# Kernel tuning notes

Measured on AMD Instinct MI355X. Metric: run time of the kernel, lower is better.

Reference implementation:

```python
import jax, jax.numpy as jnp
import numpy as np
from jax import lax

BBOX_XFORM_CLIP = float(np.log(1000.0 / 16.0))
PRE_NMS_TOP_K = 1000
SCORE_THRESH = 0.05
IOU_THRESH = 0.5
MAX_DET = 100


def _decode_boxes(encoded, anchors):
    # encoded [...,4] = [dy,dx,dh,dw] with weights [10,10,5,5]; anchors [...,4] = [y1,x1,y2,x2]
    dy = encoded[..., 0] / 10.0
    dx = encoded[..., 1] / 10.0
    dh = jnp.minimum(encoded[..., 2] / 5.0, BBOX_XFORM_CLIP)
    dw = jnp.minimum(encoded[..., 3] / 5.0, BBOX_XFORM_CLIP)
    ah = anchors[..., 2] - anchors[..., 0]
    aw = anchors[..., 3] - anchors[..., 1]
    ayc = anchors[..., 0] + 0.5 * ah
    axc = anchors[..., 1] + 0.5 * aw
    yc = dy * ah + ayc
    xc = dx * aw + axc
    h = jnp.exp(dh) * ah
    w = jnp.exp(dw) * aw
    return jnp.stack([yc - 0.5 * h, xc - 0.5 * w, yc + 0.5 * h, xc + 0.5 * w], axis=-1)


def _clip_boxes(boxes, image_shape):
    # boxes [B,N,4]; image_shape [B,2] = (height, width)
    h = image_shape[..., 0:1]
    w = image_shape[..., 1:2]
    maxlen = jnp.concatenate([h, w, h, w], axis=-1)[:, None, :]  # [B,1,4]
    return jnp.clip(boxes, 0.0, maxlen)


def _nms_keep(boxes):
    # Greedy sequential NMS on score-sorted boxes [k,4]; returns keep mask [k].
    k = boxes.shape[0]
    y1, x1, y2, x2 = boxes[:, 0], boxes[:, 1], boxes[:, 2], boxes[:, 3]
    area = (y2 - y1) * (x2 - x1)
    idxs = jnp.arange(k)

    def body(keep, i):
        iy1 = jnp.maximum(y1[i], y1)
        ix1 = jnp.maximum(x1[i], x1)
        iy2 = jnp.minimum(y2[i], y2)
        ix2 = jnp.minimum(x2[i], x2)
        inter = jnp.maximum(iy2 - iy1, 0.0) * jnp.maximum(ix2 - ix1, 0.0)
        union = area[i] + area - inter
        iou = inter / jnp.where(union > 0, union, 1.0)
        suppressed = jnp.any(keep & (idxs < i) & (iou > IOU_THRESH))
        return keep.at[i].set(~suppressed), None

    keep, _ = lax.scan(body, jnp.zeros((k,), jnp.bool_), idxs)
    return keep


def _nms_single(boxes, scores):
    # boxes [k,4], scores [k] sorted descending; mirrors sorted_non_max_suppression_padded output.
    keep = _nms_keep(lax.stop_gradient(boxes))
    valid = keep & jnp.any(boxes > 0, axis=-1)  # zeroed (filtered) boxes never count
    sel = jnp.where(valid, scores, -jnp.inf)
    top_s, top_i = lax.top_k(sel, MAX_DET)
    out_valid = top_s > -jnp.inf
    out_scores = jnp.where(out_valid, top_s, 0.0)
    out_boxes = boxes[top_i] * out_valid[:, None].astype(boxes.dtype)
    return out_scores, out_boxes


def setup_inputs() -> dict:
    key = jax.random.key(0)
    k1, k2, k3, k4 = jax.random.split(key, 4)
    B, K, C = 8, 8192, 91
    raw_boxes = jax.random.normal(k1, (B, K, C * 4), jnp.float32) * 0.5
    raw_scores = jax.random.normal(k2, (B, K, C), jnp.float32) * 2.0
    # valid anchors [y1,x1,y2,x2] inside a 1024x1024 image
    ctr = jax.random.uniform(k3, (B, K, 2), jnp.float32, 0.0, 1024.0)
    sz = jax.random.uniform(k4, (B, K, 2), jnp.float32, 16.0, 128.0)
    anchor_boxes = jnp.concatenate([ctr - 0.5 * sz, ctr + 0.5 * sz], axis=-1)
    image_shape = jnp.full((B, 2), 1024.0, jnp.float32)
    return {"raw_boxes": raw_boxes, "raw_scores": raw_scores,
            "anchor_boxes": anchor_boxes, "image_shape": image_shape}


def reference(raw_boxes, raw_scores, anchor_boxes, image_shape):
    B, K, C = raw_scores.shape
    Cc = C - 1  # background removed

    probs = jax.nn.softmax(raw_scores, axis=-1)[:, :, 1:]           # [B,K,Cc]
    boxes = raw_boxes.reshape(B, K, C, 4)[:, :, 1:, :]              # [B,K,Cc,4]
    anch = jnp.broadcast_to(anchor_boxes[:, :, None, :], boxes.shape)
    dec = _decode_boxes(boxes.reshape(B, K * Cc, 4), anch.reshape(B, K * Cc, 4))
    dec = _clip_boxes(dec, image_shape).reshape(B, K, Cc, 4)

    # per-class top-k pre-NMS candidates (_select_top_k_scores + gather)
    k = min(K, PRE_NMS_TOP_K)
    s_t = jnp.transpose(probs, (0, 2, 1))                           # [B,Cc,K]
    top_s, top_i = lax.top_k(s_t, k)                                # [B,Cc,k]
    b_t = jnp.transpose(dec, (0, 2, 1, 3))                          # [B,Cc,K,4]
    top_b = jnp.take_along_axis(b_t, top_i[..., None], axis=2)      # [B,Cc,k,4]

    # filter_boxes_by_scores: score -> -1, box -> 0 below threshold
    mask = top_s > SCORE_THRESH
    top_s = jnp.where(mask, top_s, -1.0)
    top_b = top_b * mask[..., None].astype(top_b.dtype)

    nms_s, nms_b = jax.vmap(jax.vmap(_nms_single))(top_b, top_s)    # [B,Cc,MAX_DET], [B,Cc,MAX_DET,4]
    classes = jnp.broadcast_to(jnp.arange(Cc, dtype=jnp.int32)[None, :, None], nms_s.shape)

    all_s = nms_s.reshape(B, Cc * MAX_DET)
    all_b = nms_b.reshape(B, Cc * MAX_DET, 4)
    all_c = classes.reshape(B, Cc * MAX_DET)

    fin_s, fin_i = lax.top_k(all_s, MAX_DET)
    fin_b = jnp.take_along_axis(all_b, fin_i[..., None], axis=1)
    fin_c = jnp.take_along_axis(all_c, fin_i, axis=1) + 1           # restore background offset
    num = jnp.sum((fin_s > -1.0).astype(jnp.int32), axis=1)
    return fin_b, fin_s, fin_c, num
```

## Files before the change

### kernel.cpp

```cpp
#include <hip/hip_runtime.h>
#include <stdint.h>

typedef unsigned long long ull;

#define K_ANCH   8192
#define NCLS     91
#define NCC      90
#define B_SZ     8
#define CAP      1024
#define PRE_NMS  1000
#define MAXDET   100
#define CHUNK    128
#define NWMAX    16
#define NBW      128
#define SCORE_TH 0.05f
#define IOU_TH   0.5f
#define BBOX_CLIP 4.1351665565490723f

__device__ __forceinline__ float wave_max64(float v) {
  #pragma unroll
  for (int off = 32; off > 0; off >>= 1) v = fmaxf(v, __shfl_xor(v, off, 64));
  return v;
}
__device__ __forceinline__ float wave_sum64(float v) {
  #pragma unroll
  for (int off = 32; off > 0; off >>= 1) v += __shfl_xor(v, off, 64);
  return v;
}

__device__ __forceinline__ float4 decode_clip(float4 e, float4 a, float imh, float imw) {
#pragma clang fp contract(off)
  float dy = e.x / 10.0f;
  float dx = e.y / 10.0f;
  float dh = fminf(e.z / 5.0f, BBOX_CLIP);
  float dw = fminf(e.w / 5.0f, BBOX_CLIP);
  float ah = a.z - a.x;
  float aw = a.w - a.y;
  float ayc = a.x + 0.5f * ah;
  float axc = a.y + 0.5f * aw;
  float yc = dy * ah + ayc;
  float xc = dx * aw + axc;
  float h = expf(dh) * ah;
  float w = expf(dw) * aw;
  float y1 = yc - 0.5f * h, x1 = xc - 0.5f * w;
  float y2 = yc + 0.5f * h, x2 = xc + 0.5f * w;
  y1 = fminf(fmaxf(y1, 0.0f), imh);
  x1 = fminf(fmaxf(x1, 0.0f), imw);
  y2 = fminf(fmaxf(y2, 0.0f), imh);
  x2 = fminf(fmaxf(x2, 0.0f), imw);
  return make_float4(y1, x1, y2, x2);
}

__device__ __forceinline__ bool iou_gt(float4 bi, float ai, float4 bj, float aj) {
#pragma clang fp contract(off)
  float iy1 = fmaxf(bi.x, bj.x);
  float ix1 = fmaxf(bi.y, bj.y);
  float iy2 = fminf(bi.z, bj.z);
  float ix2 = fminf(bi.w, bj.w);
  float inter = fmaxf(iy2 - iy1, 0.0f) * fmaxf(ix2 - ix1, 0.0f);
  float uni = ai + aj - inter;
  float iou = inter / (uni > 0.0f ? uni : 1.0f);
  return iou > IOU_TH;
}

__global__ __launch_bounds__(256) void kT_softmax(
    const float* __restrict__ raw_scores,
    float2* __restrict__ stats, ull* __restrict__ bmask)
{
  __shared__ ull rowbits[64][2];
  int tid = threadIdx.x;
  int wv = tid >> 6, lane = tid & 63;
  int b = blockIdx.x >> 7;
  int k0 = (blockIdx.x & 127) << 6;
  for (int i = 0; i < 16; i++) {
    int rl = (wv << 4) + i;
    int row = b * K_ANCH + k0 + rl;
    const float* srow = raw_scores + (size_t)row * NCLS;
    float s0 = srow[lane];
    bool has1 = lane < (NCLS - 64);
    float s1 = has1 ? srow[64 + lane] : -INFINITY;
    float m = wave_max64(fmaxf(s0, s1));
    float e0 = expf(s0 - m);
    float e1 = has1 ? expf(s1 - m) : 0.0f;
    float denom = wave_sum64(e0 + e1);
    ull b0 = __ballot(lane >= 1 && (e0 / denom) > SCORE_TH);
    ull b1 = __ballot(has1 && (e1 / denom) > SCORE_TH);
    if (lane == 0) {
      stats[row] = make_float2(m, denom);
      rowbits[rl][0] = b0;
      rowbits[rl][1] = b1;
    }
  }
  __syncthreads();
  if (tid < NCC) {
    int c = tid + 1, w = c >> 6, bit = c & 63;
    ull out = 0;
    for (int r = 0; r < 64; r++)
      out |= ((rowbits[r][w] >> bit) & 1ull) << r;
    bmask[(size_t)(b * NCC + tid) * NBW + (k0 >> 6)] = out;
  }
}

__global__ __launch_bounds__(256) void kN_nms(
    const float* __restrict__ raw_boxes, const float* __restrict__ raw_scores,
    const float* __restrict__ anchors, const float* __restrict__ image_shape,
    const float2* __restrict__ stats, const ull* __restrict__ bmask,
    float* __restrict__ all_s, float4* __restrict__ all_b)
{
  __shared__ ull    skey[CAP];
  __shared__ float4 sbox[PRE_NMS];
  __shared__ float  sarea[PRE_NMS];
  __shared__ ull    smask[NWMAX][CHUNK + 1];
  __shared__ int    soff[NBW];
  __shared__ int    s_n;
  __shared__ int    s_done;

  int bc  = blockIdx.x;
  int tid = threadIdx.x;
  int b = bc / NCC;
  int c = bc - b * NCC + 1;
  int outbase = bc * MAXDET;

  for (int i = tid; i < MAXDET; i += 256) {
    all_s[outbase + i] = 0.0f;
    all_b[outbase + i] = make_float4(0.f, 0.f, 0.f, 0.f);
  }

  ull w0 = 0;
  if (tid < NBW) {
    w0 = bmask[(size_t)bc * NBW + tid];
    soff[tid] = __popcll(w0);
  }
  if (tid == 0) s_done = 0;
  __syncthreads();
  if (tid == 0) {
    int acc = 0;
    for (int t = 0; t < NBW; t++) { int v = soff[t]; soff[t] = acc; acc += v; }
    s_n = acc;
  }
  __syncthreads();
  int n_load = min(s_n, CAP);

  if (tid < NBW) {
    int slot = soff[tid];
    ull m = w0;
    int kb = tid << 6;
    while (m) {
      int bit = __ffsll(m) - 1;
      m &= m - 1;
      if (slot < CAP) skey[slot] = (ull)(kb + bit);
      slot++;
    }
  }
  __syncthreads();

  size_t rowb = (size_t)b * K_ANCH;
  for (int i = tid; i < n_load; i += 256) {
    int k = (int)skey[i];
    size_t row = rowb + k;
    float s = raw_scores[row * NCLS + c];
    float2 md = stats[row];
    float p = expf(s - md.x) / md.y;
    skey[i] = ((ull)__float_as_uint(p) << 32) | (uint32_t)(K_ANCH - 1 - k);
  }
  int n2 = 256;
  while (n2 < n_load) n2 <<= 1;
  for (int i = n_load + tid; i < n2; i += 256) skey[i] = 0ull;
  __syncthreads();

  for (int size = 2; size <= n2; size <<= 1) {
    for (int stride = size >> 1; stride > 0; stride >>= 1) {
      for (int i = tid; i < n2; i += 256) {
        int j = i ^ stride;
        if (j > i) {
          ull ki = skey[i], kj = skey[j];
          bool desc = ((i & size) == 0);
          if (desc ? (ki < kj) : (ki > kj)) { skey[i] = kj; skey[j] = ki; }
        }
      }
      __syncthreads();
    }
  }

  int n_use = min(n_load, PRE_NMS);
  float imh = image_shape[b * 2 + 0];
  float imw = image_shape[b * 2 + 1];
  for (int i = tid; i < n_use; i += 256) {
    int k = K_ANCH - 1 - (int)(skey[i] & 0xFFFFFFFFull);
    size_t row = rowb + k;
    float4 e = ((const float4*)raw_boxes)[row * NCLS + c];
    float4 a = ((const float4*)anchors)[row];
    float4 box = decode_clip(e, a, imh, imw);
    sbox[i] = box;
    {
#pragma clang fp contract(off)
      sarea[i] = (box.z - box.x) * (box.w - box.y);
    }
  }

  int nwords = (n_use + 63) >> 6;
  ull rem = 0;
  int written = 0;
  for (int c0 = 0; c0 < n_use; c0 += CHUNK) {
    __syncthreads();
    if (s_done) break;
    int nrows = min(CHUNK, n_use - c0);

    for (int p = tid; p < (nwords << 7); p += 256) {
      int w  = p >> 7;
      int rr = p & (CHUNK - 1);
      if (rr >= nrows) continue;
      int r = c0 + rr;
      float4 br = sbox[r];
      float  ar = sarea[r];
      int j0 = w << 6;
      int j1 = min(j0 + 64, n_use);
      int js = max(j0, r + 1);
      ull mrow = 0;
      for (int j = js; j < j1; j++) {
        if (iou_gt(br, ar, sbox[j], sarea[j])) mrow |= 1ull << (j - j0);
      }
      smask[w][rr] = mrow;
    }
    __syncthreads();

    if (tid < 64) {
      int lane = tid;
      for (int i = c0; i < c0 + nrows; i++) {
        int w = i >> 6, bit = i & 63;
        ull rw = __shfl(rem, w, 64);
        if (((rw >> bit) & 1ull) == 0) {
          if (lane < nwords) rem |= smask[lane][i - c0];
          int valid = 0;
          float4 bx;
          float sc = 0.f;
          if (lane == 0) {
            bx = sbox[i];
            valid = (bx.x > 0.f || bx.y > 0.f || bx.z > 0.f || bx.w > 0.f) ? 1 : 0;
            sc = __uint_as_float((uint32_t)(skey[i] >> 32));
          }
          valid = __shfl(valid, 0, 64);
          if (valid) {
            if (lane == 0) {
              all_s[outbase + written] = sc;
              all_b[outbase + written] = bx;
            }
            written++;
            if (written == MAXDET) {
              if (lane == 0) s_done = 1;
              break;
            }
          }
        }
      }
    }
  }
}

__global__ __launch_bounds__(256) void k3_final(
    const float* __restrict__ all_s, const float4* __restrict__ all_b,
    float* __restrict__ out)
{
  __shared__ float ss[NCC * MAXDET];
  int b = blockIdx.x;
  int tid = threadIdx.x;
  const float* S = all_s + (size_t)b * NCC * MAXDET;
  for (int i = tid; i < NCC * MAXDET; i += 256) ss[i] = S[i];
  __syncthreads();
  if (tid >= 64) return;
  int lane = tid;

  float* fin_b = out;
  float* fin_s = out + B_SZ * MAXDET * 4;
  float* fin_c = fin_s + B_SZ * MAXDET;
  float* numo  = fin_c + B_SZ * MAXDET;

  int c0 = lane;
  int c1 = lane + 64;
  int p0 = 0, p1 = 0;
  ull k0 = ((ull)__float_as_uint(ss[c0 * MAXDET]) << 32) | (uint32_t)(16383 - c0 * MAXDET);
  ull k1 = (c1 < NCC)
         ? (((ull)__float_as_uint(ss[c1 * MAXDET]) << 32) | (uint32_t)(16383 - c1 * MAXDET))
         : 0ull;
  int cnt = 0;

  for (int step = 0; step < MAXDET; step++) {
    ull my = (k0 > k1) ? k0 : k1;
    ull g = my;
    #pragma unroll
    for (int off = 32; off > 0; off >>= 1) {
      ull o = __shfl_xor(g, off, 64);
      g = (o > g) ? o : g;
    }
    if (g == k0 && k0 != 0ull) {
      p0++;
      int flat = c0 * MAXDET + p0;
      k0 = (p0 < MAXDET)
         ? (((ull)__float_as_uint(ss[flat]) << 32) | (uint32_t)(16383 - flat))
         : 0ull;
    } else if (g == k1 && k1 != 0ull) {
      p1++;
      int flat = c1 * MAXDET + p1;
      k1 = (p1 < MAXDET)
         ? (((ull)__float_as_uint(ss[flat]) << 32) | (uint32_t)(16383 - flat))
         : 0ull;
    }

    if (lane == 0) {
      int flat = 16383 - (int)(g & 0xFFFFFFFFull);
      int cc = flat / MAXDET;
      float sc = __uint_as_float((uint32_t)(g >> 32));
      fin_s[b * MAXDET + step] = sc;
      fin_c[b * MAXDET + step] = (float)(cc + 1);
      float4 bx = all_b[(size_t)b * NCC * MAXDET + flat];
      ((float4*)fin_b)[b * MAXDET + step] = bx;
      if (sc > -1.0f) cnt++;
    }
  }
  if (lane == 0) numo[b] = (float)cnt;
}

extern "C" void kernel_launch(void* const* d_in, const int* in_sizes, int n_in,
                              void* d_out, int out_size, void* d_ws, size_t ws_size,
                              hipStream_t stream) {
  const float* raw_boxes   = (const float*)d_in[0];
  const float* raw_scores  = (const float*)d_in[1];
  const float* anchors     = (const float*)d_in[2];
  const float* image_shape = (const float*)d_in[3];

  char* p = (char*)d_ws;
  auto alloc = [&](size_t bytes) {
    char* r = p;
    p += (bytes + 255) & ~(size_t)255;
    return r;
  };
  float2* stats = (float2*)alloc((size_t)B_SZ * K_ANCH * sizeof(float2));
  ull*    bmask = (ull*)   alloc((size_t)B_SZ * NCC * NBW * sizeof(ull));
  float*  all_s = (float*) alloc((size_t)B_SZ * NCC * MAXDET * sizeof(float));
  float4* all_b = (float4*)alloc((size_t)B_SZ * NCC * MAXDET * sizeof(float4));

  kT_softmax<<<B_SZ * 128, 256, 0, stream>>>(raw_scores, stats, bmask);
  kN_nms<<<B_SZ * NCC, 256, 0, stream>>>(raw_boxes, raw_scores, anchors, image_shape,
                                         stats, bmask, all_s, all_b);
  k3_final<<<B_SZ, 256, 0, stream>>>(all_s, all_b, (float*)d_out);
}
```

Before: 310.2 us.

## Retune softmax block size, register-level bitonic sort, wave-scan offsets, smaller NMS chunks

Result: faster. 303.2 us (-2.2%).

```diff
diff --git a/kernel.cpp b/kernel.cpp
--- a/kernel.cpp
+++ b/kernel.cpp
@@ -10,7 +10,7 @@
 #define CAP      1024
 #define PRE_NMS  1000
 #define MAXDET   100
-#define CHUNK    128
+#define CHUNK    64
 #define NWMAX    16
 #define NBW      128
 #define SCORE_TH 0.05f
@@ -63,7 +63,7 @@
   return iou > IOU_TH;
 }
 
-__global__ __launch_bounds__(256) void kT_softmax(
+__global__ __launch_bounds__(1024) void kT_softmax(
     const float* __restrict__ raw_scores,
     float2* __restrict__ stats, ull* __restrict__ bmask)
 {
@@ -72,8 +72,9 @@
   int wv = tid >> 6, lane = tid & 63;
   int b = blockIdx.x >> 7;
   int k0 = (blockIdx.x & 127) << 6;
-  for (int i = 0; i < 16; i++) {
-    int rl = (wv << 4) + i;
+  #pragma unroll
+  for (int i = 0; i < 4; i++) {
+    int rl = (wv << 2) + i;
     int row = b * K_ANCH + k0 + rl;
     const float* srow = raw_scores + (size_t)row * NCLS;
     float s0 = srow[lane];
@@ -95,6 +96,7 @@
   if (tid < NCC) {
     int c = tid + 1, w = c >> 6, bit = c & 63;
     ull out = 0;
+    #pragma unroll
     for (int r = 0; r < 64; r++)
       out |= ((rowbits[r][w] >> bit) & 1ull) << r;
     bmask[(size_t)(b * NCC + tid) * NBW + (k0 >> 6)] = out;
@@ -107,13 +109,15 @@
     const float2* __restrict__ stats, const ull* __restrict__ bmask,
     float* __restrict__ all_s, float4* __restrict__ all_b)
 {
-  __shared__ ull    skey[CAP];
   __shared__ float4 sbox[PRE_NMS];
   __shared__ float  sarea[PRE_NMS];
-  __shared__ ull    smask[NWMAX][CHUNK + 1];
+  __shared__ float  sscore[PRE_NMS];
+  __shared__ ull    sbuf[1056];
   __shared__ int    soff[NBW];
+  __shared__ int    swtot[2];
   __shared__ int    s_n;
   __shared__ int    s_done;
+#define SMASK(w, r) sbuf[(w) * (CHUNK + 1) + (r)]
 
   int bc  = blockIdx.x;
   int tid = threadIdx.x;
@@ -127,17 +131,22 @@
   }
 
   ull w0 = 0;
-  if (tid < NBW) {
-    w0 = bmask[(size_t)bc * NBW + tid];
-    soff[tid] = __popcll(w0);
+  int cnt = 0;
+  if (tid < NBW) { w0 = bmask[(size_t)bc * NBW + tid]; cnt = __popcll(w0); }
+  int incl = cnt;
+  if (tid < 128) {
+    int lane = tid & 63;
+    #pragma unroll
+    for (int d = 1; d < 64; d <<= 1) {
+      int o = __shfl_up(incl, d, 64);
+      if (lane >= d) incl += o;
+    }
+    if (lane == 63) swtot[tid >> 6] = incl;
   }
   if (tid == 0) s_done = 0;
   __syncthreads();
-  if (tid == 0) {
-    int acc = 0;
-    for (int t = 0; t < NBW; t++) { int v = soff[t]; soff[t] = acc; acc += v; }
-    s_n = acc;
-  }
+  if (tid < 128) soff[tid] = incl - cnt + ((tid >= 64) ? swtot[0] : 0);
+  if (tid == 0) s_n = swtot[0] + swtot[1];
   __syncthreads();
   int n_load = min(s_n, CAP);
 
@@ -148,7 +157,7 @@
     while (m) {
       int bit = __ffsll(m) - 1;
       m &= m - 1;
-      if (slot < CAP) skey[slot] = (ull)(kb + bit);
+      if (slot < CAP) sbuf[slot] = (ull)(kb + bit);
       slot++;
     }
   }
@@ -156,29 +165,59 @@
 
   size_t rowb = (size_t)b * K_ANCH;
   for (int i = tid; i < n_load; i += 256) {
-    int k = (int)skey[i];
+    int k = (int)sbuf[i];
     size_t row = rowb + k;
     float s = raw_scores[row * NCLS + c];
     float2 md = stats[row];
     float p = expf(s - md.x) / md.y;
-    skey[i] = ((ull)__float_as_uint(p) << 32) | (uint32_t)(K_ANCH - 1 - k);
-  }
-  int n2 = 256;
-  while (n2 < n_load) n2 <<= 1;
-  for (int i = n_load + tid; i < n2; i += 256) skey[i] = 0ull;
-  __syncthreads();
-
-  for (int size = 2; size <= n2; size <<= 1) {
-    for (int stride = size >> 1; stride > 0; stride >>= 1) {
-      for (int i = tid; i < n2; i += 256) {
-        int j = i ^ stride;
-        if (j > i) {
-          ull ki = skey[i], kj = skey[j];
-          bool desc = ((i & size) == 0);
-          if (desc ? (ki < kj) : (ki > kj)) { skey[i] = kj; skey[j] = ki; }
+    sbuf[i] = ((ull)__float_as_uint(p) << 32) | (uint32_t)(K_ANCH - 1 - k);
+  }
+  int n2 = (n_load <= 512) ? 512 : 1024;
+  for (int i = n_load + tid; i < n2; i += 256) sbuf[i] = 0ull;
+  __syncthreads();
+
+  if (n_load <= 512) {
+    ull e0 = sbuf[tid], e1 = sbuf[tid + 256];
+    for (int size = 2; size <= 512; size <<= 1) {
+      if (size == 512 && e0 < e1) { ull t = e0; e0 = e1; e1 = t; }
+      for (int s = ((size >> 1) > 128 ? 128 : (size >> 1)); s >= 64; s >>= 1) {
+        __syncthreads();
+        sbuf[tid] = e0; sbuf[tid + 256] = e1;
+        __syncthreads();
+        ull p0 = sbuf[tid ^ s];
+        ull p1 = sbuf[(tid + 256) ^ s];
+        bool t0 = (((tid & s) == 0) == ((tid & size) == 0));
+        bool t1 = ((((tid + 256) & s) == 0) == (((tid + 256) & size) == 0));
+        e0 = t0 ? (e0 > p0 ? e0 : p0) : (e0 < p0 ? e0 : p0);
+        e1 = t1 ? (e1 > p1 ? e1 : p1) : (e1 < p1 ? e1 : p1);
+      }
+      int smax = ((size >> 1) < 32 ? (size >> 1) : 32);
+      for (int s = smax; s >= 1; s >>= 1) {
+        ull p0 = __shfl_xor(e0, s, 64);
+        ull p1 = __shfl_xor(e1, s, 64);
+        bool t0 = (((tid & s) == 0) == ((tid & size) == 0));
+        bool t1 = ((((tid + 256) & s) == 0) == (((tid + 256) & size) == 0));
+        e0 = t0 ? (e0 > p0 ? e0 : p0) : (e0 < p0 ? e0 : p0);
+        e1 = t1 ? (e1 > p1 ? e1 : p1) : (e1 < p1 ? e1 : p1);
+      }
+    }
+    __syncthreads();
+    sbuf[tid] = e0;
+    sbuf[tid + 256] = e1;
+    __syncthreads();
+  } else {
+    for (int size = 2; size <= 1024; size <<= 1) {
+      for (int stride = size >> 1; stride > 0; stride >>= 1) {
+        for (int i = tid; i < 1024; i += 256) {
+          int j = i ^ stride;
+          if (j > i) {
+            ull ki = sbuf[i], kj = sbuf[j];
+            bool desc = ((i & size) == 0);
+            if (desc ? (ki < kj) : (ki > kj)) { sbuf[i] = kj; sbuf[j] = ki; }
+          }
         }
-      }
-      __syncthreads();
+        __syncthreads();
+      }
     }
   }
 
@@ -186,12 +225,14 @@
   float imh = image_shape[b * 2 + 0];
   float imw = image_shape[b * 2 + 1];
   for (int i = tid; i < n_use; i += 256) {
-    int k = K_ANCH - 1 - (int)(skey[i] & 0xFFFFFFFFull);
+    ull key = sbuf[i];
+    int k = K_ANCH - 1 - (int)(key & 0xFFFFFFFFull);
     size_t row = rowb + k;
     float4 e = ((const float4*)raw_boxes)[row * NCLS + c];
     float4 a = ((const float4*)anchors)[row];
     float4 box = decode_clip(e, a, imh, imw);
     sbox[i] = box;
+    sscore[i] = __uint_as_float((uint32_t)(key >> 32));
     {
 #pragma clang fp contract(off)
       sarea[i] = (box.z - box.x) * (box.w - box.y);
@@ -206,8 +247,8 @@
     if (s_done) break;
     int nrows = min(CHUNK, n_use - c0);
 
-    for (int p = tid; p < (nwords << 7); p += 256) {
-      int w  = p >> 7;
+    for (int p = tid; p < (nwords << 6); p += 256) {
+      int w  = p >> 6;
       int rr = p & (CHUNK - 1);
       if (rr >= nrows) continue;
       int r = c0 + rr;
@@ -220,7 +261,7 @@
       for (int j = js; j < j1; j++) {
         if (iou_gt(br, ar, sbox[j], sarea[j])) mrow |= 1ull << (j - j0);
       }
-      smask[w][rr] = mrow;
+      SMASK(w, rr) = mrow;
     }
     __syncthreads();
 
@@ -230,14 +271,14 @@
         int w = i >> 6, bit = i & 63;
         ull rw = __shfl(rem, w, 64);
         if (((rw >> bit) & 1ull) == 0) {
-          if (lane < nwords) rem |= smask[lane][i - c0];
+          if (lane < nwords) rem |= SMASK(lane, i - c0);
           int valid = 0;
           float4 bx;
           float sc = 0.f;
           if (lane == 0) {
             bx = sbox[i];
             valid = (bx.x > 0.f || bx.y > 0.f || bx.z > 0.f || bx.w > 0.f) ? 1 : 0;
-            sc = __uint_as_float((uint32_t)(skey[i] >> 32));
+            sc = sscore[i];
           }
           valid = __shfl(valid, 0, 64);
           if (valid) {
@@ -255,6 +296,7 @@
       }
     }
   }
+#undef SMASK
 }
 
 __global__ __launch_bounds__(256) void k3_final(
@@ -278,32 +320,35 @@
   int c0 = lane;
   int c1 = lane + 64;
   int p0 = 0, p1 = 0;
-  ull k0 = ((ull)__float_as_uint(ss[c0 * MAXDET]) << 32) | (uint32_t)(16383 - c0 * MAXDET);
-  ull k1 = (c1 < NCC)
-         ? (((ull)__float_as_uint(ss[c1 * MAXDET]) << 32) | (uint32_t)(16383 - c1 * MAXDET))
-         : 0ull;
+  ull cur0 = ((ull)__float_as_uint(ss[c0 * MAXDET]) << 32) | (uint32_t)(16383 - c0 * MAXDET);
+  ull nxt0 = ((ull)__float_as_uint(ss[c0 * MAXDET + 1]) << 32) | (uint32_t)(16383 - (c0 * MAXDET + 1));
+  ull cur1 = 0ull, nxt1 = 0ull;
+  if (c1 < NCC) {
+    cur1 = ((ull)__float_as_uint(ss[c1 * MAXDET]) << 32) | (uint32_t)(16383 - c1 * MAXDET);
+    nxt1 = ((ull)__float_as_uint(ss[c1 * MAXDET + 1]) << 32) | (uint32_t)(16383 - (c1 * MAXDET + 1));
+  }
   int cnt = 0;
 
   for (int step = 0; step < MAXDET; step++) {
-    ull my = (k0 > k1) ? k0 : k1;
+    ull my = (cur0 > cur1) ? cur0 : cur1;
     ull g = my;
     #pragma unroll
     for (int off = 32; off > 0; off >>= 1) {
       ull o = __shfl_xor(g, off, 64);
       g = (o > g) ? o : g;
     }
-    if (g == k0 && k0 != 0ull) {
+    if (cur0 != 0ull && g == cur0) {
       p0++;
-      int flat = c0 * MAXDET + p0;
-      k0 = (p0 < MAXDET)
-         ? (((ull)__float_as_uint(ss[flat]) << 32) | (uint32_t)(16383 - flat))
-         : 0ull;
-    } else if (g == k1 && k1 != 0ull) {
+      cur0 = nxt0;
+      int f = c0 * MAXDET + p0 + 1;
+      nxt0 = (p0 + 1 < MAXDET)
+           ? (((ull)__float_as_uint(ss[f]) << 32) | (uint32_t)(16383 - f)) : 0ull;
+    } else if (cur1 != 0ull && g == cur1) {
       p1++;
-      int flat = c1 * MAXDET + p1;
-      k1 = (p1 < MAXDET)
-         ? (((ull)__float_as_uint(ss[flat]) << 32) | (uint32_t)(16383 - flat))
-         : 0ull;
+      cur1 = nxt1;
+      int f = c1 * MAXDET + p1 + 1;
+      nxt1 = (p1 + 1 < MAXDET)
+           ? (((ull)__float_as_uint(ss[f]) << 32) | (uint32_t)(16383 - f)) : 0ull;
     }
 
     if (lane == 0) {
@@ -339,7 +384,7 @@
   float*  all_s = (float*) alloc((size_t)B_SZ * NCC * MAXDET * sizeof(float));
   float4* all_b = (float4*)alloc((size_t)B_SZ * NCC * MAXDET * sizeof(float4));
 
-  kT_softmax<<<B_SZ * 128, 256, 0, stream>>>(raw_scores, stats, bmask);
+  kT_softmax<<<B_SZ * 128, 1024, 0, stream>>>(raw_scores, stats, bmask);
   kN_nms<<<B_SZ * NCC, 256, 0, stream>>>(raw_boxes, raw_scores, anchors, image_shape,
                                          stats, bmask, all_s, all_b);
   k3_final<<<B_SZ, 256, 0, stream>>>(all_s, all_b, (float*)d_out);
```
